# Kernel optimization log

Measured on AMD Instinct MI355X. Metric: run time of the kernel, lower is better.

The kernel has to match this reference:

```python
import jax, jax.numpy as jnp
import numpy as np

IN_CH = 64
HIDDEN_CH = 256

def setup_inputs() -> dict:
    key = jax.random.key(0)
    k = jax.random.split(key, 8)
    za = jax.random.normal(k[0], (8, 256, IN_CH), dtype=jnp.float32)
    zb = jax.random.normal(k[1], (8, 256, IN_CH), dtype=jnp.float32)
    # 1x1 conv weights stored as (out_ch, in_ch); biases zero per torch init
    w0 = jax.random.normal(k[2], (HIDDEN_CH, IN_CH), dtype=jnp.float32) * 0.05
    b0 = jnp.zeros((HIDDEN_CH,), dtype=jnp.float32)
    w1 = jax.random.normal(k[3], (HIDDEN_CH, HIDDEN_CH), dtype=jnp.float32) * 0.05
    b1 = jnp.zeros((HIDDEN_CH,), dtype=jnp.float32)
    w2 = jax.random.normal(k[4], (1, HIDDEN_CH), dtype=jnp.float32) * 0.05
    b2 = jnp.zeros((1,), dtype=jnp.float32)
    return {"za": za, "zb": zb, "w0": w0, "b0": b0, "w1": w1, "b1": b1, "w2": w2, "b2": b2}

def _leaky_relu(x):
    return jnp.where(x >= 0, x, 0.01 * x)  # torch LeakyReLU default slope

def reference(za, zb, w0, b0, w1, b1, w2, b2):
    # z_dif: (N, A, B, C) pairwise broadcast difference (channel-last; 1x1 conv = per-pixel linear)
    z_dif = za[:, :, None, :] - zb[:, None, :, :]
    y = _leaky_relu(jnp.einsum('nabc,hc->nabh', z_dif, w0) + b0)
    y = _leaky_relu(jnp.einsum('nabh,gh->nabg', y, w1) + b1)
    y = jax.nn.sigmoid(jnp.einsum('nabh,oh->nabo', y, w2) + b2)
    return y[..., 0]  # (N, A, B)
```

## Files before the change

kernel.cpp:

```cpp
#include <hip/hip_runtime.h>
#include <hip/hip_fp16.h>


typedef float f32x16 __attribute__((ext_vector_type(16)));
typedef _Float16 f16x8 __attribute__((ext_vector_type(8)));
typedef int i32x4 __attribute__((ext_vector_type(4)));

__global__ __launch_bounds__(256) void pack_all(
    const float* __restrict__ za, const float* __restrict__ zb,
    const float* __restrict__ w0, const float* __restrict__ b0,
    const float* __restrict__ w1,
    _Float16* __restrict__ upack, _Float16* __restrict__ vpack,
    _Float16* __restrict__ vlin, _Float16* __restrict__ w1pk) {
  int bid = blockIdx.x;
  int tid = threadIdx.x;
  if (bid < 2048) {
    int nr = bid;
    int n = nr >> 8, r = nr & 255;
    __shared__ float arow[64], brow[64];
    if (tid < 64) arow[tid] = za[nr * 64 + tid];
    else if (tid < 128) brow[tid - 64] = zb[nr * 64 + (tid - 64)];
    __syncthreads();
    int h = tid;
    const float* w0r = w0 + h * 64;
    float ua = 0.f, vb = 0.f;
#pragma unroll
    for (int c = 0; c < 64; c += 4) {
      float4 w = *reinterpret_cast<const float4*>(w0r + c);
      ua += w.x * arow[c] + w.y * arow[c + 1] + w.z * arow[c + 2] + w.w * arow[c + 3];
      vb += w.x * brow[c] + w.y * brow[c + 1] + w.z * brow[c + 2] + w.w * brow[c + 3];
    }
    upack[nr * 256 + h] = (_Float16)(ua + b0[h]);
    _Float16 vh = (_Float16)vb;
    vlin[nr * 256 + h] = vh;
    int bblk = r >> 5, lcol = r & 31;
    int kiter = h >> 4, rem = h & 15, lh = rem >> 3, j = rem & 7;
    int lane = lh * 32 + lcol;
    vpack[(((n * 8 + bblk) * 16 + kiter) * 64 + lane) * 8 + j] = vh;
  } else {
    int id = (bid - 2048) * 256 + tid;
    int g = id >> 8, k = id & 255;
    int gt = g >> 5, lcol = g & 31;
    int kiter = k >> 4, rem = k & 15, lh = rem >> 3, j = rem & 7;
    int lane = lh * 32 + lcol;
    w1pk[((kiter * 8 + gt) * 64 + lane) * 8 + j] = (_Float16)(0.495f * w1[id]);
  }
}

__global__ __launch_bounds__(256) void pq_kernel(
    const _Float16* __restrict__ upack, const _Float16* __restrict__ vlin,
    const float* __restrict__ w1, const float* __restrict__ b1,
    float* __restrict__ Ra, float* __restrict__ Sb) {
  int bid = blockIdx.x;
  int which = bid >> 9;
  int nr0 = (bid & 511) * 4;
  __shared__ float rows[4][256];
  int tid = threadIdx.x;
  const _Float16* src = which ? vlin : upack;
#pragma unroll
  for (int i = 0; i < 4; ++i)
    rows[i][tid] = (float)src[(size_t)(nr0 + i) * 256 + tid];
  __syncthreads();
  int g = tid;
  const float* w1r = w1 + (size_t)g * 256;
  float acc0 = 0.f, acc1 = 0.f, acc2 = 0.f, acc3 = 0.f;
#pragma unroll 8
  for (int k = 0; k < 256; k += 4) {
    float4 w = *reinterpret_cast<const float4*>(w1r + k);
    acc0 += w.x * rows[0][k] + w.y * rows[0][k + 1] + w.z * rows[0][k + 2] + w.w * rows[0][k + 3];
    acc1 += w.x * rows[1][k] + w.y * rows[1][k + 1] + w.z * rows[1][k + 2] + w.w * rows[1][k + 3];
    acc2 += w.x * rows[2][k] + w.y * rows[2][k + 1] + w.z * rows[2][k + 2] + w.w * rows[2][k + 3];
    acc3 += w.x * rows[3][k] + w.y * rows[3][k + 1] + w.z * rows[3][k + 2] + w.w * rows[3][k + 3];
  }
  if (which == 0) {
    float bb = b1[g];
    Ra[(size_t)(nr0 + 0) * 256 + g] = 0.505f * acc0 + bb;
    Ra[(size_t)(nr0 + 1) * 256 + g] = 0.505f * acc1 + bb;
    Ra[(size_t)(nr0 + 2) * 256 + g] = 0.505f * acc2 + bb;
    Ra[(size_t)(nr0 + 3) * 256 + g] = 0.505f * acc3 + bb;
  } else {
    Sb[(size_t)(nr0 + 0) * 256 + g] = 0.505f * acc0;
    Sb[(size_t)(nr0 + 1) * 256 + g] = 0.505f * acc1;
    Sb[(size_t)(nr0 + 2) * 256 + g] = 0.505f * acc2;
    Sb[(size_t)(nr0 + 3) * 256 + g] = 0.505f * acc3;
  }
}

template <int MODE>
__global__ __launch_bounds__(512, 2) void fused_main(
    const _Float16* __restrict__ upack, const _Float16* __restrict__ vpack,
    const _Float16* __restrict__ w1pk,
    const float* __restrict__ Ra, const float* __restrict__ Sb,
    const float* __restrict__ w2, const float* __restrict__ b2,
    float* __restrict__ pws, float* __restrict__ out) {
  int bid = blockIdx.x;
  int n = bid >> 6;
  int bblk = (bid >> 3) & 7;
  int aq = bid & 7;
  int tid = threadIdx.x;
  int ws = tid >> 6;
  int l = tid & 63;
  int l31 = l & 31, lh = l >> 5;

  f16x8 w1f[16];
#pragma unroll
  for (int kt = 0; kt < 16; ++kt)
    w1f[kt] = *reinterpret_cast<const f16x8*>(w1pk + ((kt * 8 + ws) * 64 + l) * 8);

  const _Float16* vbase = vpack + (size_t)((n * 8 + bblk) * 16) * 512 + l * 8;
  f16x8 vf[16];
#pragma unroll
  for (int kt = 0; kt < 16; ++kt)
    vf[kt] = *reinterpret_cast<const f16x8*>(vbase + kt * 512);

  float sbf[16], w2f[16];
  const float* sbrow = Sb + (size_t)(n * 256 + bblk * 32 + l31) * 256;
#pragma unroll
  for (int rg = 0; rg < 4; ++rg) {
    int gbase = ws * 32 + 8 * rg + 4 * lh;
    float4 ss = *reinterpret_cast<const float4*>(sbrow + gbase);
    float4 ww = *reinterpret_cast<const float4*>(w2 + gbase);
    sbf[4 * rg + 0] = ss.x; sbf[4 * rg + 1] = ss.y;
    sbf[4 * rg + 2] = ss.z; sbf[4 * rg + 3] = ss.w;
    w2f[4 * rg + 0] = ww.x; w2f[4 * rg + 1] = ww.y;
    w2f[4 * rg + 2] = ww.z; w2f[4 * rg + 3] = ww.w;
  }
  float b2v = b2[0];

  const _Float16* ub = upack + (size_t)(n * 256 + aq * 32) * 256 + lh * 8;
  const float* rabase = Ra + (size_t)(n * 256 + aq * 32) * 256;

  if constexpr (MODE == 0) {
    float* pw = pws + ((size_t)bid * 32 * 8 + ws) * 32;
    for (int it = 0; it < 32; it += 2) {
      const _Float16* ur0 = ub + (size_t)it * 256;
      const _Float16* ur1 = ur0 + 256;
      const float* rar0 = rabase + (size_t)it * 256;
      const float* rar1 = rar0 + 256;

      f32x16 acc0, acc1;
#pragma unroll
      for (int rg = 0; rg < 4; ++rg) {
        float4 r0 = *reinterpret_cast<const float4*>(rar0 + ws * 32 + 8 * rg + 4 * lh);
        float4 r1 = *reinterpret_cast<const float4*>(rar1 + ws * 32 + 8 * rg + 4 * lh);
        acc0[4 * rg + 0] = r0.x - sbf[4 * rg + 0];
        acc0[4 * rg + 1] = r0.y - sbf[4 * rg + 1];
        acc0[4 * rg + 2] = r0.z - sbf[4 * rg + 2];
        acc0[4 * rg + 3] = r0.w - sbf[4 * rg + 3];
        acc1[4 * rg + 0] = r1.x - sbf[4 * rg + 0];
        acc1[4 * rg + 1] = r1.y - sbf[4 * rg + 1];
        acc1[4 * rg + 2] = r1.z - sbf[4 * rg + 2];
        acc1[4 * rg + 3] = r1.w - sbf[4 * rg + 3];
      }

#pragma unroll
      for (int kt = 0; kt < 16; ++kt) {
        f16x8 u0 = *reinterpret_cast<const f16x8*>(ur0 + kt * 16);
        f16x8 u1 = *reinterpret_cast<const f16x8*>(ur1 + kt * 16);
        f16x8 d0 = u0 - vf[kt];
        f16x8 d1 = u1 - vf[kt];
        i32x4 i0 = __builtin_bit_cast(i32x4, d0); i0 &= 0x7fff7fff;
        i32x4 i1 = __builtin_bit_cast(i32x4, d1); i1 &= 0x7fff7fff;
        acc0 = __builtin_amdgcn_mfma_f32_32x32x16_f16(
            w1f[kt], __builtin_bit_cast(f16x8, i0), acc0, 0, 0, 0);
        acc1 = __builtin_amdgcn_mfma_f32_32x32x16_f16(
            w1f[kt], __builtin_bit_cast(f16x8, i1), acc1, 0, 0, 0);
      }

      float q00 = 0.f, q01 = 0.f, q02 = 0.f, q03 = 0.f;
      float q10 = 0.f, q11 = 0.f, q12 = 0.f, q13 = 0.f;
#pragma unroll
      for (int rg = 0; rg < 4; ++rg) {
        float h;
        h = acc0[4 * rg + 0]; h = fmaxf(h, 0.01f * h); q00 = fmaf(h, w2f[4 * rg + 0], q00);
        h = acc0[4 * rg + 1]; h = fmaxf(h, 0.01f * h); q01 = fmaf(h, w2f[4 * rg + 1], q01);
        h = acc0[4 * rg + 2]; h = fmaxf(h, 0.01f * h); q02 = fmaf(h, w2f[4 * rg + 2], q02);
        h = acc0[4 * rg + 3]; h = fmaxf(h, 0.01f * h); q03 = fmaf(h, w2f[4 * rg + 3], q03);
        h = acc1[4 * rg + 0]; h = fmaxf(h, 0.01f * h); q10 = fmaf(h, w2f[4 * rg + 0], q10);
        h = acc1[4 * rg + 1]; h = fmaxf(h, 0.01f * h); q11 = fmaf(h, w2f[4 * rg + 1], q11);
        h = acc1[4 * rg + 2]; h = fmaxf(h, 0.01f * h); q12 = fmaf(h, w2f[4 * rg + 2], q12);
        h = acc1[4 * rg + 3]; h = fmaxf(h, 0.01f * h); q13 = fmaf(h, w2f[4 * rg + 3], q13);
      }
      float p0 = (q00 + q01) + (q02 + q03);
      float p1 = (q10 + q11) + (q12 + q13);
      p0 += __shfl_xor(p0, 32, 64);
      p1 += __shfl_xor(p1, 32, 64);
      if (l < 32) {
        pw[(size_t)it * 256 + l31] = p0;
        pw[(size_t)(it + 1) * 256 + l31] = p1;
      }
    }
  } else {
    __shared__ float lds_p[2][4][8][32];
    for (int bt = 0; bt < 8; ++bt) {
      int ph = bt & 1;
      for (int j = 0; j < 4; ++j) {
        int it = bt * 4 + j;
        const _Float16* ur = ub + (size_t)it * 256;
        const float* rar = rabase + (size_t)it * 256;

        f32x16 accA;
#pragma unroll
        for (int rg = 0; rg < 4; ++rg) {
          float4 rr = *reinterpret_cast<const float4*>(rar + ws * 32 + 8 * rg + 4 * lh);
          accA[4 * rg + 0] = rr.x - sbf[4 * rg + 0];
          accA[4 * rg + 1] = rr.y - sbf[4 * rg + 1];
          accA[4 * rg + 2] = rr.z - sbf[4 * rg + 2];
          accA[4 * rg + 3] = rr.w - sbf[4 * rg + 3];
        }
#pragma unroll
        for (int kt = 0; kt < 16; ++kt) {
          f16x8 uu = *reinterpret_cast<const f16x8*>(ur + kt * 16);
          f16x8 d = uu - vf[kt];
          i32x4 di = __builtin_bit_cast(i32x4, d);
          di &= 0x7fff7fff;
          accA = __builtin_amdgcn_mfma_f32_32x32x16_f16(
              w1f[kt], __builtin_bit_cast(f16x8, di), accA, 0, 0, 0);
        }
        float p = 0.f;
#pragma unroll
        for (int r = 0; r < 16; ++r) {
          float s = accA[r];
          float h = fmaxf(s, 0.01f * s);
          p = fmaf(h, w2f[r], p);
        }
        p += __shfl_xor(p, 32, 64);
        if (l < 32) lds_p[ph][j][ws][l31] = p;
      }
      __syncthreads();
      if (tid < 128) {
        int al = tid >> 5, b = tid & 31;
        float s = b2v;
#pragma unroll
        for (int w = 0; w < 8; ++w) s += lds_p[ph][al][w][b];
        int a = aq * 32 + bt * 4 + al;
        out[(size_t)(n * 256 + a) * 256 + bblk * 32 + b] = 1.f / (1.f + __expf(-s));
      }
    }
  }
}

__global__ __launch_bounds__(256) void reduce_kernel(
    const float* __restrict__ pws, const float* __restrict__ b2,
    float* __restrict__ out) {
  int o = blockIdx.x * 256 + threadIdx.x;
  int n = o >> 16, a = (o >> 8) & 255, b = o & 255;
  int bblk = b >> 5, b32 = b & 31, aq = a >> 5, it = a & 31;
  int mbid = (n << 6) | (bblk << 3) | aq;
  const float* p = pws + (((size_t)mbid * 32 + it) * 8) * 32 + b32;
  float s = b2[0];
#pragma unroll
  for (int w = 0; w < 8; ++w) s += p[w * 32];
  out[o] = 1.f / (1.f + __expf(-s));
}

extern "C" void kernel_launch(void* const* d_in, const int* in_sizes, int n_in,
                              void* d_out, int out_size, void* d_ws, size_t ws_size,
                              hipStream_t stream) {
  const float* za = (const float*)d_in[0];
  const float* zb = (const float*)d_in[1];
  const float* w0 = (const float*)d_in[2];
  const float* b0 = (const float*)d_in[3];
  const float* w1 = (const float*)d_in[4];
  const float* b1 = (const float*)d_in[5];
  const float* w2 = (const float*)d_in[6];
  const float* b2 = (const float*)d_in[7];
  float* out = (float*)d_out;

  char* ws = (char*)d_ws;
  _Float16* upack = (_Float16*)ws;
  _Float16* vpack = (_Float16*)(ws + (1u << 20));
  _Float16* vlin  = (_Float16*)(ws + (2u << 20));
  _Float16* w1pk  = (_Float16*)(ws + (3u << 20));
  float*    Ra    = (float*)(ws + (7u << 19));
  float*    Sb    = (float*)(ws + (11u << 19));
  float*    pws   = (float*)(ws + (15u << 19));

  pack_all<<<2304, 256, 0, stream>>>(za, zb, w0, b0, w1, upack, vpack, vlin, w1pk);
  pq_kernel<<<1024, 256, 0, stream>>>(upack, vlin, w1, b1, Ra, Sb);

  const size_t need = (15ull << 19) + 512ull * 32 * 8 * 32 * 4;
  if (ws_size >= need) {
    fused_main<0><<<512, 512, 0, stream>>>(upack, vpack, w1pk, Ra, Sb, w2, b2, pws, out);
    reduce_kernel<<<2048, 256, 0, stream>>>(pws, b2, out);
  } else {
    fused_main<1><<<512, 512, 0, stream>>>(upack, vpack, w1pk, Ra, Sb, w2, b2, nullptr, out);
  }
}
```

Measured before the change: 170.6 us.

## Fuse pq into pack kernel; split main kernel into 256-thread blocks with LDS v

Folds the per-row W1 projections (Ra, Sb) into the pack kernel, removing one kernel launch and the vlin buffer. The main kernel now uses 256-thread blocks that each cover half of the hidden channels (twice as many blocks). The v fragments are staged in LDS instead of registers, and Sb, Ra and w2 are loaded inside the epilogue rather than kept resident. The aim is lower register pressure and higher occupancy, paid for with extra LDS reads per iteration, fewer rows per block in the pack kernel's second GEMV, and only one MFMA chain per iteration instead of two.

```diff
diff --git a/kernel.cpp b/kernel.cpp
--- a/kernel.cpp
+++ b/kernel.cpp
@@ -9,15 +9,17 @@
 __global__ __launch_bounds__(256) void pack_all(
     const float* __restrict__ za, const float* __restrict__ zb,
     const float* __restrict__ w0, const float* __restrict__ b0,
-    const float* __restrict__ w1,
+    const float* __restrict__ w1, const float* __restrict__ b1,
     _Float16* __restrict__ upack, _Float16* __restrict__ vpack,
-    _Float16* __restrict__ vlin, _Float16* __restrict__ w1pk) {
+    _Float16* __restrict__ w1pk,
+    float* __restrict__ Ra, float* __restrict__ Sb) {
   int bid = blockIdx.x;
   int tid = threadIdx.x;
   if (bid < 2048) {
     int nr = bid;
     int n = nr >> 8, r = nr & 255;
     __shared__ float arow[64], brow[64];
+    __shared__ float ulds[256], vlds[256];
     if (tid < 64) arow[tid] = za[nr * 64 + tid];
     else if (tid < 128) brow[tid - 64] = zb[nr * 64 + (tid - 64)];
     __syncthreads();
@@ -30,213 +32,107 @@
       ua += w.x * arow[c] + w.y * arow[c + 1] + w.z * arow[c + 2] + w.w * arow[c + 3];
       vb += w.x * brow[c] + w.y * brow[c + 1] + w.z * brow[c + 2] + w.w * brow[c + 3];
     }
-    upack[nr * 256 + h] = (_Float16)(ua + b0[h]);
+    _Float16 uh = (_Float16)(ua + b0[h]);
     _Float16 vh = (_Float16)vb;
-    vlin[nr * 256 + h] = vh;
+    upack[nr * 256 + h] = uh;
     int bblk = r >> 5, lcol = r & 31;
-    int kiter = h >> 4, rem = h & 15, lh = rem >> 3, j = rem & 7;
-    int lane = lh * 32 + lcol;
-    vpack[(((n * 8 + bblk) * 16 + kiter) * 64 + lane) * 8 + j] = vh;
+    int kiter = h >> 4, rem = h & 15, lh2 = rem >> 3, j = rem & 7;
+    vpack[(((n * 8 + bblk) * 16 + kiter) * 64 + lh2 * 32 + lcol) * 8 + j] = vh;
+    ulds[h] = (float)uh;
+    vlds[h] = (float)vh;
+    __syncthreads();
+    int g = tid;
+    const float* w1r = w1 + (size_t)g * 256;
+    float au = 0.f, av = 0.f;
+#pragma unroll 8
+    for (int k = 0; k < 256; k += 4) {
+      float4 w = *reinterpret_cast<const float4*>(w1r + k);
+      au += w.x * ulds[k] + w.y * ulds[k + 1] + w.z * ulds[k + 2] + w.w * ulds[k + 3];
+      av += w.x * vlds[k] + w.y * vlds[k + 1] + w.z * vlds[k + 2] + w.w * vlds[k + 3];
+    }
+    Ra[(size_t)nr * 256 + g] = 0.505f * au + b1[g];
+    Sb[(size_t)nr * 256 + g] = 0.505f * av;
   } else {
     int id = (bid - 2048) * 256 + tid;
     int g = id >> 8, k = id & 255;
     int gt = g >> 5, lcol = g & 31;
-    int kiter = k >> 4, rem = k & 15, lh = rem >> 3, j = rem & 7;
-    int lane = lh * 32 + lcol;
-    w1pk[((kiter * 8 + gt) * 64 + lane) * 8 + j] = (_Float16)(0.495f * w1[id]);
-  }
-}
-
-__global__ __launch_bounds__(256) void pq_kernel(
-    const _Float16* __restrict__ upack, const _Float16* __restrict__ vlin,
-    const float* __restrict__ w1, const float* __restrict__ b1,
-    float* __restrict__ Ra, float* __restrict__ Sb) {
-  int bid = blockIdx.x;
-  int which = bid >> 9;
-  int nr0 = (bid & 511) * 4;
-  __shared__ float rows[4][256];
-  int tid = threadIdx.x;
-  const _Float16* src = which ? vlin : upack;
-#pragma unroll
-  for (int i = 0; i < 4; ++i)
-    rows[i][tid] = (float)src[(size_t)(nr0 + i) * 256 + tid];
-  __syncthreads();
-  int g = tid;
-  const float* w1r = w1 + (size_t)g * 256;
-  float acc0 = 0.f, acc1 = 0.f, acc2 = 0.f, acc3 = 0.f;
-#pragma unroll 8
-  for (int k = 0; k < 256; k += 4) {
-    float4 w = *reinterpret_cast<const float4*>(w1r + k);
-    acc0 += w.x * rows[0][k] + w.y * rows[0][k + 1] + w.z * rows[0][k + 2] + w.w * rows[0][k + 3];
-    acc1 += w.x * rows[1][k] + w.y * rows[1][k + 1] + w.z * rows[1][k + 2] + w.w * rows[1][k + 3];
-    acc2 += w.x * rows[2][k] + w.y * rows[2][k + 1] + w.z * rows[2][k + 2] + w.w * rows[2][k + 3];
-    acc3 += w.x * rows[3][k] + w.y * rows[3][k + 1] + w.z * rows[3][k + 2] + w.w * rows[3][k + 3];
-  }
-  if (which == 0) {
-    float bb = b1[g];
-    Ra[(size_t)(nr0 + 0) * 256 + g] = 0.505f * acc0 + bb;
-    Ra[(size_t)(nr0 + 1) * 256 + g] = 0.505f * acc1 + bb;
-    Ra[(size_t)(nr0 + 2) * 256 + g] = 0.505f * acc2 + bb;
-    Ra[(size_t)(nr0 + 3) * 256 + g] = 0.505f * acc3 + bb;
-  } else {
-    Sb[(size_t)(nr0 + 0) * 256 + g] = 0.505f * acc0;
-    Sb[(size_t)(nr0 + 1) * 256 + g] = 0.505f * acc1;
-    Sb[(size_t)(nr0 + 2) * 256 + g] = 0.505f * acc2;
-    Sb[(size_t)(nr0 + 3) * 256 + g] = 0.505f * acc3;
-  }
-}
-
-template <int MODE>
-__global__ __launch_bounds__(512, 2) void fused_main(
+    int kiter = k >> 4, rem = k & 15, lh2 = rem >> 3, j = rem & 7;
+    w1pk[((kiter * 8 + gt) * 64 + lh2 * 32 + lcol) * 8 + j] = (_Float16)(0.495f * w1[id]);
+  }
+}
+
+__global__ __launch_bounds__(256, 4) void fused_main(
     const _Float16* __restrict__ upack, const _Float16* __restrict__ vpack,
     const _Float16* __restrict__ w1pk,
     const float* __restrict__ Ra, const float* __restrict__ Sb,
-    const float* __restrict__ w2, const float* __restrict__ b2,
-    float* __restrict__ pws, float* __restrict__ out) {
+    const float* __restrict__ w2, float* __restrict__ pws) {
+  __shared__ _Float16 vsh[8192];
   int bid = blockIdx.x;
-  int n = bid >> 6;
-  int bblk = (bid >> 3) & 7;
-  int aq = bid & 7;
+  int gh = bid & 1;
+  int mbid = bid >> 1;
+  int aq = mbid & 7;
+  int bblk = (mbid >> 3) & 7;
+  int n = mbid >> 6;
   int tid = threadIdx.x;
   int ws = tid >> 6;
+  int gt = gh * 4 + ws;
   int l = tid & 63;
   int l31 = l & 31, lh = l >> 5;
 
+  {
+    const f16x8* vsrc = reinterpret_cast<const f16x8*>(
+        vpack + (size_t)((n * 8 + bblk) * 16) * 512);
+    f16x8* vdst = reinterpret_cast<f16x8*>(vsh);
+    vdst[tid] = vsrc[tid];
+    vdst[tid + 256] = vsrc[tid + 256];
+    vdst[tid + 512] = vsrc[tid + 512];
+    vdst[tid + 768] = vsrc[tid + 768];
+  }
   f16x8 w1f[16];
 #pragma unroll
   for (int kt = 0; kt < 16; ++kt)
-    w1f[kt] = *reinterpret_cast<const f16x8*>(w1pk + ((kt * 8 + ws) * 64 + l) * 8);
-
-  const _Float16* vbase = vpack + (size_t)((n * 8 + bblk) * 16) * 512 + l * 8;
-  f16x8 vf[16];
-#pragma unroll
-  for (int kt = 0; kt < 16; ++kt)
-    vf[kt] = *reinterpret_cast<const f16x8*>(vbase + kt * 512);
-
-  float sbf[16], w2f[16];
+    w1f[kt] = *reinterpret_cast<const f16x8*>(w1pk + ((kt * 8 + gt) * 64 + l) * 8);
+  __syncthreads();
+
+  const _Float16* ub = upack + (size_t)(n * 256 + aq * 32) * 256 + lh * 8;
+  const float* rab = Ra + (size_t)(n * 256 + aq * 32) * 256;
   const float* sbrow = Sb + (size_t)(n * 256 + bblk * 32 + l31) * 256;
-#pragma unroll
-  for (int rg = 0; rg < 4; ++rg) {
-    int gbase = ws * 32 + 8 * rg + 4 * lh;
-    float4 ss = *reinterpret_cast<const float4*>(sbrow + gbase);
-    float4 ww = *reinterpret_cast<const float4*>(w2 + gbase);
-    sbf[4 * rg + 0] = ss.x; sbf[4 * rg + 1] = ss.y;
-    sbf[4 * rg + 2] = ss.z; sbf[4 * rg + 3] = ss.w;
-    w2f[4 * rg + 0] = ww.x; w2f[4 * rg + 1] = ww.y;
-    w2f[4 * rg + 2] = ww.z; w2f[4 * rg + 3] = ww.w;
-  }
-  float b2v = b2[0];
-
-  const _Float16* ub = upack + (size_t)(n * 256 + aq * 32) * 256 + lh * 8;
-  const float* rabase = Ra + (size_t)(n * 256 + aq * 32) * 256;
-
-  if constexpr (MODE == 0) {
-    float* pw = pws + ((size_t)bid * 32 * 8 + ws) * 32;
-    for (int it = 0; it < 32; it += 2) {
-      const _Float16* ur0 = ub + (size_t)it * 256;
-      const _Float16* ur1 = ur0 + 256;
-      const float* rar0 = rabase + (size_t)it * 256;
-      const float* rar1 = rar0 + 256;
-
-      f32x16 acc0, acc1;
-#pragma unroll
-      for (int rg = 0; rg < 4; ++rg) {
-        float4 r0 = *reinterpret_cast<const float4*>(rar0 + ws * 32 + 8 * rg + 4 * lh);
-        float4 r1 = *reinterpret_cast<const float4*>(rar1 + ws * 32 + 8 * rg + 4 * lh);
-        acc0[4 * rg + 0] = r0.x - sbf[4 * rg + 0];
-        acc0[4 * rg + 1] = r0.y - sbf[4 * rg + 1];
-        acc0[4 * rg + 2] = r0.z - sbf[4 * rg + 2];
-        acc0[4 * rg + 3] = r0.w - sbf[4 * rg + 3];
-        acc1[4 * rg + 0] = r1.x - sbf[4 * rg + 0];
-        acc1[4 * rg + 1] = r1.y - sbf[4 * rg + 1];
-        acc1[4 * rg + 2] = r1.z - sbf[4 * rg + 2];
-        acc1[4 * rg + 3] = r1.w - sbf[4 * rg + 3];
-      }
-
-#pragma unroll
-      for (int kt = 0; kt < 16; ++kt) {
-        f16x8 u0 = *reinterpret_cast<const f16x8*>(ur0 + kt * 16);
-        f16x8 u1 = *reinterpret_cast<const f16x8*>(ur1 + kt * 16);
-        f16x8 d0 = u0 - vf[kt];
-        f16x8 d1 = u1 - vf[kt];
-        i32x4 i0 = __builtin_bit_cast(i32x4, d0); i0 &= 0x7fff7fff;
-        i32x4 i1 = __builtin_bit_cast(i32x4, d1); i1 &= 0x7fff7fff;
-        acc0 = __builtin_amdgcn_mfma_f32_32x32x16_f16(
-            w1f[kt], __builtin_bit_cast(f16x8, i0), acc0, 0, 0, 0);
-        acc1 = __builtin_amdgcn_mfma_f32_32x32x16_f16(
-            w1f[kt], __builtin_bit_cast(f16x8, i1), acc1, 0, 0, 0);
-      }
-
-      float q00 = 0.f, q01 = 0.f, q02 = 0.f, q03 = 0.f;
-      float q10 = 0.f, q11 = 0.f, q12 = 0.f, q13 = 0.f;
-#pragma unroll
-      for (int rg = 0; rg < 4; ++rg) {
-        float h;
-        h = acc0[4 * rg + 0]; h = fmaxf(h, 0.01f * h); q00 = fmaf(h, w2f[4 * rg + 0], q00);
-        h = acc0[4 * rg + 1]; h = fmaxf(h, 0.01f * h); q01 = fmaf(h, w2f[4 * rg + 1], q01);
-        h = acc0[4 * rg + 2]; h = fmaxf(h, 0.01f * h); q02 = fmaf(h, w2f[4 * rg + 2], q02);
-        h = acc0[4 * rg + 3]; h = fmaxf(h, 0.01f * h); q03 = fmaf(h, w2f[4 * rg + 3], q03);
-        h = acc1[4 * rg + 0]; h = fmaxf(h, 0.01f * h); q10 = fmaf(h, w2f[4 * rg + 0], q10);
-        h = acc1[4 * rg + 1]; h = fmaxf(h, 0.01f * h); q11 = fmaf(h, w2f[4 * rg + 1], q11);
-        h = acc1[4 * rg + 2]; h = fmaxf(h, 0.01f * h); q12 = fmaf(h, w2f[4 * rg + 2], q12);
-        h = acc1[4 * rg + 3]; h = fmaxf(h, 0.01f * h); q13 = fmaf(h, w2f[4 * rg + 3], q13);
-      }
-      float p0 = (q00 + q01) + (q02 + q03);
-      float p1 = (q10 + q11) + (q12 + q13);
-      p0 += __shfl_xor(p0, 32, 64);
-      p1 += __shfl_xor(p1, 32, 64);
-      if (l < 32) {
-        pw[(size_t)it * 256 + l31] = p0;
-        pw[(size_t)(it + 1) * 256 + l31] = p1;
-      }
-    }
-  } else {
-    __shared__ float lds_p[2][4][8][32];
-    for (int bt = 0; bt < 8; ++bt) {
-      int ph = bt & 1;
-      for (int j = 0; j < 4; ++j) {
-        int it = bt * 4 + j;
-        const _Float16* ur = ub + (size_t)it * 256;
-        const float* rar = rabase + (size_t)it * 256;
-
-        f32x16 accA;
-#pragma unroll
-        for (int rg = 0; rg < 4; ++rg) {
-          float4 rr = *reinterpret_cast<const float4*>(rar + ws * 32 + 8 * rg + 4 * lh);
-          accA[4 * rg + 0] = rr.x - sbf[4 * rg + 0];
-          accA[4 * rg + 1] = rr.y - sbf[4 * rg + 1];
-          accA[4 * rg + 2] = rr.z - sbf[4 * rg + 2];
-          accA[4 * rg + 3] = rr.w - sbf[4 * rg + 3];
-        }
-#pragma unroll
-        for (int kt = 0; kt < 16; ++kt) {
-          f16x8 uu = *reinterpret_cast<const f16x8*>(ur + kt * 16);
-          f16x8 d = uu - vf[kt];
-          i32x4 di = __builtin_bit_cast(i32x4, d);
-          di &= 0x7fff7fff;
-          accA = __builtin_amdgcn_mfma_f32_32x32x16_f16(
-              w1f[kt], __builtin_bit_cast(f16x8, di), accA, 0, 0, 0);
-        }
-        float p = 0.f;
-#pragma unroll
-        for (int r = 0; r < 16; ++r) {
-          float s = accA[r];
-          float h = fmaxf(s, 0.01f * s);
-          p = fmaf(h, w2f[r], p);
-        }
-        p += __shfl_xor(p, 32, 64);
-        if (l < 32) lds_p[ph][j][ws][l31] = p;
-      }
-      __syncthreads();
-      if (tid < 128) {
-        int al = tid >> 5, b = tid & 31;
-        float s = b2v;
-#pragma unroll
-        for (int w = 0; w < 8; ++w) s += lds_p[ph][al][w][b];
-        int a = aq * 32 + bt * 4 + al;
-        out[(size_t)(n * 256 + a) * 256 + bblk * 32 + b] = 1.f / (1.f + __expf(-s));
-      }
-    }
+  float* pw = pws + ((size_t)(mbid * 32) * 8 + gh * 4 + ws) * 32;
+
+  for (int it = 0; it < 32; ++it) {
+    const _Float16* ur = ub + (size_t)it * 256;
+
+    f32x16 acc;
+#pragma unroll
+    for (int r = 0; r < 16; ++r) acc[r] = 0.f;
+
+#pragma unroll
+    for (int kt = 0; kt < 16; ++kt) {
+      f16x8 uu = *reinterpret_cast<const f16x8*>(ur + kt * 16);
+      f16x8 vv = *reinterpret_cast<const f16x8*>(vsh + kt * 512 + l * 8);
+      f16x8 d = uu - vv;
+      i32x4 di = __builtin_bit_cast(i32x4, d);
+      di &= 0x7fff7fff;
+      acc = __builtin_amdgcn_mfma_f32_32x32x16_f16(
+          w1f[kt], __builtin_bit_cast(f16x8, di), acc, 0, 0, 0);
+    }
+
+    const float* rar = rab + (size_t)it * 256;
+    float p = 0.f;
+#pragma unroll
+    for (int rg = 0; rg < 4; ++rg) {
+      int gb = gt * 32 + 8 * rg + 4 * lh;
+      float4 rr = *reinterpret_cast<const float4*>(rar + gb);
+      float4 ss = *reinterpret_cast<const float4*>(sbrow + gb);
+      float4 ww = *reinterpret_cast<const float4*>(w2 + gb);
+      float s, h;
+      s = acc[4 * rg + 0] + rr.x - ss.x; h = fmaxf(s, 0.01f * s); p = fmaf(h, ww.x, p);
+      s = acc[4 * rg + 1] + rr.y - ss.y; h = fmaxf(s, 0.01f * s); p = fmaf(h, ww.y, p);
+      s = acc[4 * rg + 2] + rr.z - ss.z; h = fmaxf(s, 0.01f * s); p = fmaf(h, ww.z, p);
+      s = acc[4 * rg + 3] + rr.w - ss.w; h = fmaxf(s, 0.01f * s); p = fmaf(h, ww.w, p);
+    }
+    p += __shfl_xor(p, 32, 64);
+    if (l < 32) pw[(size_t)it * 256 + l31] = p;
   }
 }
 
@@ -252,6 +148,95 @@
 #pragma unroll
   for (int w = 0; w < 8; ++w) s += p[w * 32];
   out[o] = 1.f / (1.f + __expf(-s));
+}
+
+__global__ __launch_bounds__(512, 2) void fused_fb(
+    const _Float16* __restrict__ upack, const _Float16* __restrict__ vpack,
+    const _Float16* __restrict__ w1pk,
+    const float* __restrict__ Ra, const float* __restrict__ Sb,
+    const float* __restrict__ w2, const float* __restrict__ b2,
+    float* __restrict__ out) {
+  __shared__ float lds_p[2][4][8][32];
+  int bid = blockIdx.x;
+  int n = bid >> 6;
+  int bblk = (bid >> 3) & 7;
+  int aq = bid & 7;
+  int tid = threadIdx.x;
+  int ws = tid >> 6;
+  int l = tid & 63;
+  int l31 = l & 31, lh = l >> 5;
+
+  f16x8 w1f[16];
+#pragma unroll
+  for (int kt = 0; kt < 16; ++kt)
+    w1f[kt] = *reinterpret_cast<const f16x8*>(w1pk + ((kt * 8 + ws) * 64 + l) * 8);
+  const _Float16* vbase = vpack + (size_t)((n * 8 + bblk) * 16) * 512 + l * 8;
+  f16x8 vf[16];
+#pragma unroll
+  for (int kt = 0; kt < 16; ++kt)
+    vf[kt] = *reinterpret_cast<const f16x8*>(vbase + kt * 512);
+
+  float sbf[16], w2f[16];
+  const float* sbrow = Sb + (size_t)(n * 256 + bblk * 32 + l31) * 256;
+#pragma unroll
+  for (int rg = 0; rg < 4; ++rg) {
+    int gbase = ws * 32 + 8 * rg + 4 * lh;
+    float4 ss = *reinterpret_cast<const float4*>(sbrow + gbase);
+    float4 ww = *reinterpret_cast<const float4*>(w2 + gbase);
+    sbf[4 * rg + 0] = ss.x; sbf[4 * rg + 1] = ss.y;
+    sbf[4 * rg + 2] = ss.z; sbf[4 * rg + 3] = ss.w;
+    w2f[4 * rg + 0] = ww.x; w2f[4 * rg + 1] = ww.y;
+    w2f[4 * rg + 2] = ww.z; w2f[4 * rg + 3] = ww.w;
+  }
+  float b2v = b2[0];
+
+  const _Float16* ub = upack + (size_t)(n * 256 + aq * 32) * 256 + lh * 8;
+  const float* rabase = Ra + (size_t)(n * 256 + aq * 32) * 256;
+
+  for (int bt = 0; bt < 8; ++bt) {
+    int ph = bt & 1;
+    for (int j = 0; j < 4; ++j) {
+      int it = bt * 4 + j;
+      const _Float16* ur = ub + (size_t)it * 256;
+      const float* rar = rabase + (size_t)it * 256;
+      f32x16 accA;
+#pragma unroll
+      for (int rg = 0; rg < 4; ++rg) {
+        float4 rr = *reinterpret_cast<const float4*>(rar + ws * 32 + 8 * rg + 4 * lh);
+        accA[4 * rg + 0] = rr.x - sbf[4 * rg + 0];
+        accA[4 * rg + 1] = rr.y - sbf[4 * rg + 1];
+        accA[4 * rg + 2] = rr.z - sbf[4 * rg + 2];
+        accA[4 * rg + 3] = rr.w - sbf[4 * rg + 3];
+      }
+#pragma unroll
+      for (int kt = 0; kt < 16; ++kt) {
+        f16x8 uu = *reinterpret_cast<const f16x8*>(ur + kt * 16);
+        f16x8 d = uu - vf[kt];
+        i32x4 di = __builtin_bit_cast(i32x4, d);
+        di &= 0x7fff7fff;
+        accA = __builtin_amdgcn_mfma_f32_32x32x16_f16(
+            w1f[kt], __builtin_bit_cast(f16x8, di), accA, 0, 0, 0);
+      }
+      float p = 0.f;
+#pragma unroll
+      for (int r = 0; r < 16; ++r) {
+        float s = accA[r];
+        float h = fmaxf(s, 0.01f * s);
+        p = fmaf(h, w2f[r], p);
+      }
+      p += __shfl_xor(p, 32, 64);
+      if (l < 32) lds_p[ph][j][ws][l31] = p;
+    }
+    __syncthreads();
+    if (tid < 128) {
+      int al = tid >> 5, b = tid & 31;
+      float s = b2v;
+#pragma unroll
+      for (int w = 0; w < 8; ++w) s += lds_p[ph][al][w][b];
+      int a = aq * 32 + bt * 4 + al;
+      out[(size_t)(n * 256 + a) * 256 + bblk * 32 + b] = 1.f / (1.f + __expf(-s));
+    }
+  }
 }
 
 extern "C" void kernel_launch(void* const* d_in, const int* in_sizes, int n_in,
@@ -270,20 +255,19 @@
   char* ws = (char*)d_ws;
   _Float16* upack = (_Float16*)ws;
   _Float16* vpack = (_Float16*)(ws + (1u << 20));
-  _Float16* vlin  = (_Float16*)(ws + (2u << 20));
-  _Float16* w1pk  = (_Float16*)(ws + (3u << 20));
-  float*    Ra    = (float*)(ws + (7u << 19));
-  float*    Sb    = (float*)(ws + (11u << 19));
-  float*    pws   = (float*)(ws + (15u << 19));
-
-  pack_all<<<2304, 256, 0, stream>>>(za, zb, w0, b0, w1, upack, vpack, vlin, w1pk);
-  pq_kernel<<<1024, 256, 0, stream>>>(upack, vlin, w1, b1, Ra, Sb);
-
-  const size_t need = (15ull << 19) + 512ull * 32 * 8 * 32 * 4;
+  _Float16* w1pk  = (_Float16*)(ws + (2u << 20));
+  float*    Ra    = (float*)(ws + (4u << 20));
+  float*    Sb    = (float*)(ws + (6u << 20));
+  float*    pws   = (float*)(ws + (8u << 20));
+
+  pack_all<<<2304, 256, 0, stream>>>(za, zb, w0, b0, w1, b1,
+                                     upack, vpack, w1pk, Ra, Sb);
+
+  const size_t need = (24ull << 20);
   if (ws_size >= need) {
-    fused_main<0><<<512, 512, 0, stream>>>(upack, vpack, w1pk, Ra, Sb, w2, b2, pws, out);
+    fused_main<<<1024, 256, 0, stream>>>(upack, vpack, w1pk, Ra, Sb, w2, pws);
     reduce_kernel<<<2048, 256, 0, stream>>>(pws, b2, out);
   } else {
-    fused_main<1><<<512, 512, 0, stream>>>(upack, vpack, w1pk, Ra, Sb, w2, b2, nullptr, out);
-  }
-}
+    fused_fb<<<512, 512, 0, stream>>>(upack, vpack, w1pk, Ra, Sb, w2, b2, out);
+  }
+}
```

Result: slower. 415.2 us (+143.3%).
